# Optimization experiments

Hardware: AMD Instinct MI355X
Metric: run time of the kernel (lower is better)

Reference implementation:

```python
import jax, jax.numpy as jnp
import numpy as np

N_NODES = 100000


def _sage_conv(x, src, dst, W_l, b_l, W_r):
    # mean-aggregate neighbor (source) features at target nodes
    gathered = x[src]                                   # [E, D]
    summed = jax.ops.segment_sum(gathered, dst, num_segments=N_NODES)  # [N, D]
    deg = jax.ops.segment_sum(jnp.ones((src.shape[0],), x.dtype), dst,
                              num_segments=N_NODES)     # [N]
    mean = summed / jnp.maximum(deg, 1.0)[:, None]      # zero stays zero for isolated nodes
    # PyG SAGEConv: lin_l(aggr) + lin_r(x); bias on lin_l only
    return mean @ W_l + b_l + x @ W_r


def setup_inputs() -> dict:
    key = jax.random.key(0)
    ks = jax.random.split(key, 9)
    x = jax.random.normal(ks[0], (N_NODES, 128), dtype=jnp.float32)
    edge_index = jax.random.randint(ks[1], (2, 1600000), 0, N_NODES, dtype=jnp.int64)
    s1 = 1.0 / np.sqrt(128.0)
    s2 = 1.0 / np.sqrt(32.0)
    return {
        "x": x,
        "edge_index": edge_index,
        "W1_l": jax.random.normal(ks[2], (128, 32), jnp.float32) * s1,
        "b1_l": jax.random.normal(ks[3], (32,), jnp.float32) * s1,
        "W1_r": jax.random.normal(ks[4], (128, 32), jnp.float32) * s1,
        "W2_l": jax.random.normal(ks[5], (32, 32), jnp.float32) * s2,
        "b2_l": jax.random.normal(ks[6], (32,), jnp.float32) * s2,
        "W2_r": jax.random.normal(ks[7], (32, 32), jnp.float32) * s2,
    }


def reference(x, edge_index, W1_l, b1_l, W1_r, W2_l, b2_l, W2_r):
    src, dst = edge_index[0], edge_index[1]
    h = _sage_conv(x, src, dst, W1_l, b1_l, W1_r)
    h = jax.nn.relu(h)
    # dropout is identity in eval mode
    h = _sage_conv(h, src, dst, W2_l, b2_l, W2_r)
    return jax.nn.relu(h)
```

## Files before the change

### kernel.cpp

```cpp
#include <hip/hip_runtime.h>


typedef _Float16 f16;
typedef _Float16 f16x2 __attribute__((ext_vector_type(2)));
typedef _Float16 f16x4 __attribute__((ext_vector_type(4)));
typedef _Float16 half8 __attribute__((ext_vector_type(8)));
typedef float f32x4 __attribute__((ext_vector_type(4)));

#define MAXBINS 2048
#define SHIFT 6
#define BINSZ 64
#define CAP 48
#define GSC 256
#define BSC 512
#define SRC_BITS 17
#define SRC_MASK 0x1FFFFu
#define XSTRIDE 136


__global__ __launch_bounds__(BSC) void block_hist(const int* __restrict__ dst,
                                                  int* __restrict__ blockHist,
                                                  int E, int chunk) {
    __shared__ int sh[MAXBINS];
    for (int i = threadIdx.x; i < MAXBINS; i += BSC) sh[i] = 0;
    __syncthreads();
    int base = blockIdx.x * chunk;
    int end = base + chunk < E ? base + chunk : E;
    for (int e = base + threadIdx.x; e < end; e += BSC)
        atomicAdd(&sh[dst[e] >> SHIFT], 1);
    __syncthreads();
    for (int i = threadIdx.x; i < MAXBINS; i += BSC)
        blockHist[(size_t)blockIdx.x * MAXBINS + i] = sh[i];
}

__global__ __launch_bounds__(256) void col_scan(const int* __restrict__ blockHist,
                                                int* __restrict__ blockBaseRel,
                                                int* __restrict__ binTot) {
    const int wave = threadIdx.x >> 6;
    const int lane = threadIdx.x & 63;
    const int bin = blockIdx.x * 4 + wave;
    int carry = 0;
#pragma unroll
    for (int r = 0; r < GSC / 64; ++r) {
        int b = r * 64 + lane;
        int v = blockHist[(size_t)b * MAXBINS + bin];
        int inc = v;
#pragma unroll
        for (int off = 1; off < 64; off <<= 1) {
            int t = __shfl_up(inc, off, 64);
            if (lane >= off) inc += t;
        }
        blockBaseRel[(size_t)b * MAXBINS + bin] = carry + (inc - v);
        carry += __shfl(inc, 63, 64);
    }
    binTot[bin] = carry;
}

__global__ __launch_bounds__(1024) void scan_bins(const int* __restrict__ binTot,
                                                  int* __restrict__ binStart,
                                                  int* __restrict__ binCnt) {
    __shared__ int sh[1024];
    int t = threadIdx.x;
    int v0 = binTot[2 * t], v1 = binTot[2 * t + 1];
    sh[t] = v0 + v1;
    __syncthreads();
    for (int off = 1; off < 1024; off <<= 1) {
        int x = 0;
        if (t >= off) x = sh[t - off];
        __syncthreads();
        sh[t] += x;
        __syncthreads();
    }
    int excl = sh[t] - (v0 + v1);
    binStart[2 * t] = excl;
    binStart[2 * t + 1] = excl + v0;
    binCnt[2 * t] = v0;
    binCnt[2 * t + 1] = v1;
}

__global__ __launch_bounds__(BSC) void scatter_binned(const int* __restrict__ src,
                                                      const int* __restrict__ dst,
                                                      const int* __restrict__ blockBaseRel,
                                                      const int* __restrict__ binStart,
                                                      unsigned* __restrict__ pairs,
                                                      int E, int chunk) {
    __shared__ int cur[MAXBINS];
    for (int i = threadIdx.x; i < MAXBINS; i += BSC)
        cur[i] = blockBaseRel[(size_t)blockIdx.x * MAXBINS + i] + binStart[i];
    __syncthreads();
    int base = blockIdx.x * chunk;
    int end = base + chunk < E ? base + chunk : E;
    for (int e = base + threadIdx.x; e < end; e += BSC) {
        int s = src[e], d = dst[e];
        int slot = atomicAdd(&cur[d >> SHIFT], 1);
        pairs[slot] = ((unsigned)(d & (BINSZ - 1)) << SRC_BITS) | (unsigned)s;
    }
}


__global__ __launch_bounds__(256) void gemm_mfma(const float* __restrict__ x,
                                                 const float* __restrict__ Wl,
                                                 const float* __restrict__ Wr,
                                                 f16* __restrict__ yl,
                                                 float* __restrict__ yr,
                                                 int N) {
    __shared__ f16 sX[64 * XSTRIDE];
    __shared__ f16 sWT[64 * XSTRIDE];
    const int tid = threadIdx.x;
    const int row0 = blockIdx.x * 64;

    for (int i = tid; i < 64 * 32; i += 256) {
        int r = i >> 5, c4 = i & 31;
        int row = row0 + r;
        float4 v = make_float4(0.f, 0.f, 0.f, 0.f);
        if (row < N) v = *(const float4*)(x + (size_t)row * 128 + c4 * 4);
        f16* d = &sX[r * XSTRIDE + c4 * 4];
        d[0] = (f16)v.x; d[1] = (f16)v.y; d[2] = (f16)v.z; d[3] = (f16)v.w;
    }
    for (int i = tid; i < 64 * 128; i += 256) {
        int k = i >> 6, n = i & 63;
        float v = (n < 32) ? Wl[k * 32 + n] : Wr[k * 32 + (n - 32)];
        sWT[n * XSTRIDE + k] = (f16)v;
    }
    __syncthreads();

    const int w = tid >> 6;
    const int lane = tid & 63;
    const int l15 = lane & 15, quad = lane >> 4;
    f32x4 acc[4] = {};
#pragma unroll
    for (int kc = 0; kc < 4; ++kc) {
        half8 af = *(const half8*)&sX[(w * 16 + l15) * XSTRIDE + kc * 32 + quad * 8];
#pragma unroll
        for (int nt = 0; nt < 4; ++nt) {
            half8 bf = *(const half8*)&sWT[(nt * 16 + l15) * XSTRIDE + kc * 32 + quad * 8];
            acc[nt] = __builtin_amdgcn_mfma_f32_16x16x32_f16(af, bf, acc[nt], 0, 0, 0);
        }
    }
#pragma unroll
    for (int nt = 0; nt < 4; ++nt) {
        int c = nt * 16 + l15;
#pragma unroll
        for (int r = 0; r < 4; ++r) {
            int g = row0 + w * 16 + quad * 4 + r;
            if (g < N) {
                if (c < 32) yl[(size_t)g * 32 + c] = (f16)acc[nt][r];
                else        yr[(size_t)g * 32 + (c - 32)] = acc[nt][r];
            }
        }
    }
}


__device__ __forceinline__ void pull_pair(const int* sBucket, int n0, int n1,
                                          int m0, int m1,
                                          const f16x2* __restrict__ y2, int col2,
                                          float2* r0, float2* r1) {
    const int4* bk0 = (const int4*)&sBucket[n0 * CAP];
    const int4* bk1 = (const int4*)&sBucket[n1 * CAP];
    float a0x = 0.f, a0y = 0.f, a1x = 0.f, a1y = 0.f;
    const int q0 = m0 >> 2, q1 = m1 >> 2;
    const int qmax = q0 > q1 ? q0 : q1;
    for (int j = 0; j < qmax; ++j) {
        if (j < q0) {
            int4 a = bk0[j];
            f16x2 v0 = y2[(size_t)a.x * 16 + col2];
            f16x2 v1 = y2[(size_t)a.y * 16 + col2];
            f16x2 v2 = y2[(size_t)a.z * 16 + col2];
            f16x2 v3 = y2[(size_t)a.w * 16 + col2];
            a0x += ((float)v0[0] + (float)v1[0]) + ((float)v2[0] + (float)v3[0]);
            a0y += ((float)v0[1] + (float)v1[1]) + ((float)v2[1] + (float)v3[1]);
        }
        if (j < q1) {
            int4 a = bk1[j];
            f16x2 v0 = y2[(size_t)a.x * 16 + col2];
            f16x2 v1 = y2[(size_t)a.y * 16 + col2];
            f16x2 v2 = y2[(size_t)a.z * 16 + col2];
            f16x2 v3 = y2[(size_t)a.w * 16 + col2];
            a1x += ((float)v0[0] + (float)v1[0]) + ((float)v2[0] + (float)v3[0]);
            a1y += ((float)v0[1] + (float)v1[1]) + ((float)v2[1] + (float)v3[1]);
        }
    }
    for (int jj = q0 * 4; jj < m0; ++jj) {
        int s = sBucket[n0 * CAP + jj];
        f16x2 v = y2[(size_t)s * 16 + col2];
        a0x += (float)v[0]; a0y += (float)v[1];
    }
    for (int jj = q1 * 4; jj < m1; ++jj) {
        int s = sBucket[n1 * CAP + jj];
        f16x2 v = y2[(size_t)s * 16 + col2];
        a1x += (float)v[0]; a1y += (float)v[1];
    }
    *r0 = make_float2(a0x, a0y);
    *r1 = make_float2(a1x, a1y);
}

__global__ __launch_bounds__(256) void agg_l1(const unsigned* __restrict__ pairs,
                                              const int* __restrict__ binStart,
                                              const int* __restrict__ binCnt,
                                              const f16* __restrict__ yl,
                                              const float* __restrict__ yr,
                                              const float* __restrict__ b1,
                                              const float* __restrict__ W2l,
                                              const float* __restrict__ W2r,
                                              f16* __restrict__ zl,
                                              float* __restrict__ zr,
                                              int N) {
    __shared__ int sBucket[BINSZ * CAP];
    __shared__ int sCnt[BINSZ];
    __shared__ float sW[2048];
    __shared__ float sB[32];
    const int tid = threadIdx.x;
    if (tid < BINSZ) sCnt[tid] = 0;
    if (tid < 32) sB[tid] = b1[tid];
    for (int i = tid; i < 2048; i += 256) sW[i] = (i < 1024) ? W2l[i] : W2r[i - 1024];
    __syncthreads();

    const int b = blockIdx.x;
    const int start = binStart[b];
    const int endE = start + binCnt[b];
    for (int e = start + tid; e < endE; e += 256) {
        unsigned pk = pairs[e];
        int local = pk >> SRC_BITS;
        int slot = atomicAdd(&sCnt[local], 1);
        if (slot < CAP) sBucket[local * CAP + slot] = (int)(pk & SRC_MASK);
    }
    __syncthreads();

    const int grp = tid >> 4;
    const int col2 = tid & 15;
    const int node0 = b << SHIFT;
    const f16x2* yl2 = (const f16x2*)yl;
    const float2 bb = *(const float2*)&sB[2 * col2];

    int deg[4], mm[4];
#pragma unroll
    for (int it = 0; it < 4; ++it) {
        deg[it] = sCnt[grp + it * 16];
        mm[it] = deg[it] < CAP ? deg[it] : CAP;
    }
    float2 acc[4];
    pull_pair(sBucket, grp, grp + 32, mm[0], mm[2], yl2, col2, &acc[0], &acc[2]);
    pull_pair(sBucket, grp + 16, grp + 48, mm[1], mm[3], yl2, col2, &acc[1], &acc[3]);

    float2 hreg[4];
#pragma unroll
    for (int it = 0; it < 4; ++it) {
        int g = node0 + grp + it * 16;
        float2 hv = make_float2(0.f, 0.f);
        if (g < N) {
            float dg = deg[it] > 1 ? (float)deg[it] : 1.0f;
            float2 loc = *(const float2*)(yr + (size_t)g * 32 + 2 * col2);
            hv.x = fmaxf(acc[it].x / dg + bb.x + loc.x, 0.0f);
            hv.y = fmaxf(acc[it].y / dg + bb.y + loc.y, 0.0f);
        }
        hreg[it] = hv;
    }
    __syncthreads();

    float* sH = (float*)sBucket;
#pragma unroll
    for (int it = 0; it < 4; ++it) {
        int n = grp + it * 16;
        *(float2*)&sH[n * 34 + 2 * col2] = hreg[it];
    }
    __syncthreads();

    const int n2 = tid >> 3;
    const int cq = tid & 7;
    const float4* sW4l = (const float4*)sW;
    const float4* sW4r = (const float4*)(sW + 1024);
#pragma unroll
    for (int it = 0; it < 2; ++it) {
        int n = it * 32 + n2;
        int g = node0 + n;
        float4 al = make_float4(0.f, 0.f, 0.f, 0.f);
        float4 ar = make_float4(0.f, 0.f, 0.f, 0.f);
#pragma unroll 8
        for (int k = 0; k < 32; ++k) {
            float hk = sH[n * 34 + k];
            float4 wl = sW4l[k * 8 + cq];
            float4 wr = sW4r[k * 8 + cq];
            al.x += hk * wl.x; al.y += hk * wl.y; al.z += hk * wl.z; al.w += hk * wl.w;
            ar.x += hk * wr.x; ar.y += hk * wr.y; ar.z += hk * wr.z; ar.w += hk * wr.w;
        }
        if (g < N) {
            f16x4 h;
            h[0] = (f16)al.x; h[1] = (f16)al.y; h[2] = (f16)al.z; h[3] = (f16)al.w;
            *(f16x4*)(zl + (size_t)g * 32 + cq * 4) = h;
            *(float4*)(zr + (size_t)g * 32 + cq * 4) = ar;
        }
    }
}

__global__ __launch_bounds__(256) void agg_l2(const unsigned* __restrict__ pairs,
                                              const int* __restrict__ binStart,
                                              const int* __restrict__ binCnt,
                                              const f16* __restrict__ zl,
                                              const float* __restrict__ b2,
                                              float* __restrict__ io,
                                              int N) {
    __shared__ int sBucket[BINSZ * CAP];
    __shared__ int sCnt[BINSZ];
    __shared__ float sB[32];
    const int tid = threadIdx.x;
    if (tid < BINSZ) sCnt[tid] = 0;
    if (tid < 32) sB[tid] = b2[tid];
    __syncthreads();

    const int b = blockIdx.x;
    const int start = binStart[b];
    const int endE = start + binCnt[b];
    for (int e = start + tid; e < endE; e += 256) {
        unsigned pk = pairs[e];
        int local = pk >> SRC_BITS;
        int slot = atomicAdd(&sCnt[local], 1);
        if (slot < CAP) sBucket[local * CAP + slot] = (int)(pk & SRC_MASK);
    }
    __syncthreads();

    const int grp = tid >> 4, col2 = tid & 15;
    const int node0 = b << SHIFT;
    const f16x2* zl2 = (const f16x2*)zl;
    const float2 bb = *(const float2*)&sB[2 * col2];

    int deg[4], mm[4];
#pragma unroll
    for (int it = 0; it < 4; ++it) {
        deg[it] = sCnt[grp + it * 16];
        mm[it] = deg[it] < CAP ? deg[it] : CAP;
    }
    float2 acc[4];
    pull_pair(sBucket, grp, grp + 32, mm[0], mm[2], zl2, col2, &acc[0], &acc[2]);
    pull_pair(sBucket, grp + 16, grp + 48, mm[1], mm[3], zl2, col2, &acc[1], &acc[3]);

#pragma unroll
    for (int it = 0; it < 4; ++it) {
        int g = node0 + grp + it * 16;
        if (g >= N) continue;
        float dg = deg[it] > 1 ? (float)deg[it] : 1.0f;
        float2 io2 = *(const float2*)(io + (size_t)g * 32 + 2 * col2);
        float2 o;
        o.x = fmaxf(acc[it].x / dg + bb.x + io2.x, 0.0f);
        o.y = fmaxf(acc[it].y / dg + bb.y + io2.y, 0.0f);
        *(float2*)(io + (size_t)g * 32 + 2 * col2) = o;
    }
}

extern "C" void kernel_launch(void* const* d_in, const int* in_sizes, int n_in,
                              void* d_out, int out_size, void* d_ws, size_t ws_size,
                              hipStream_t stream) {
    const float* x    = (const float*)d_in[0];
    const int*   ei   = (const int*)d_in[1];
    const float* W1l  = (const float*)d_in[2];
    const float* b1l  = (const float*)d_in[3];
    const float* W1r  = (const float*)d_in[4];
    const float* W2l  = (const float*)d_in[5];
    const float* b2l  = (const float*)d_in[6];
    const float* W2r  = (const float*)d_in[7];

    const int N = in_sizes[0] / 128;
    const int E = in_sizes[1] / 2;
    const int* srcIdx = ei;
    const int* dstIdx = ei + E;

    const int nbins = (N + BINSZ - 1) >> SHIFT;
    const int chunk = (E + GSC - 1) / GSC;

    int*      blockHist = (int*)d_ws;
    int*      blockBase = blockHist + (size_t)GSC * MAXBINS;
    int*      binTot    = blockBase + (size_t)GSC * MAXBINS;
    int*      binStart  = binTot + MAXBINS;
    int*      binCnt    = binStart + MAXBINS;
    unsigned* pairs     = (unsigned*)(binCnt + MAXBINS);
    f16*      A         = (f16*)(pairs + E);
    float*    B         = (float*)(A + (size_t)N * 32);
    f16*      Z         = (f16*)(B + (size_t)N * 32);
    float*    outp      = (float*)d_out;

    block_hist<<<GSC, BSC, 0, stream>>>(dstIdx, blockHist, E, chunk);
    col_scan<<<MAXBINS / 4, 256, 0, stream>>>(blockHist, blockBase, binTot);
    scan_bins<<<1, 1024, 0, stream>>>(binTot, binStart, binCnt);
    scatter_binned<<<GSC, BSC, 0, stream>>>(srcIdx, dstIdx, blockBase, binStart,
                                            pairs, E, chunk);

    gemm_mfma<<<(N + 63) / 64, 256, 0, stream>>>(x, W1l, W1r, A, B, N);
    agg_l1<<<nbins, 256, 0, stream>>>(pairs, binStart, binCnt, A, B, b1l,
                                      W2l, W2r, Z, outp, N);
    agg_l2<<<nbins, 256, 0, stream>>>(pairs, binStart, binCnt, Z, b2l, outp, N);
}
```

Baseline: 223.4 us.

## Gather 16-byte neighbor rows per thread with padded buckets and sentinel row

The aggregation kernels now assign four threads per node. Each thread loads half8 (16-byte) slices of neighbor rows, replacing the earlier 16 threads per node each loading 4-byte f16x2 values. Buckets are padded to multiples of 8 with a sentinel index N, which points at an extra padded row allocated past the end of the intermediate buffers, so the inner loop has no tail handling. The GEMM grid is enlarged so that it writes the padded rows, and some bounds checks are dropped. This cuts the number of memory instructions and the per-edge overhead, but relies on padded rows being finite. It also lowers the number of threads in flight per node.

```diff
diff --git a/kernel.cpp b/kernel.cpp
--- a/kernel.cpp
+++ b/kernel.cpp
@@ -11,6 +11,7 @@
 #define SHIFT 6
 #define BINSZ 64
 #define CAP 48
+#define BSTR 52
 #define GSC 256
 #define BSC 512
 #define SRC_BITS 17
@@ -143,57 +144,12 @@
 #pragma unroll
         for (int r = 0; r < 4; ++r) {
             int g = row0 + w * 16 + quad * 4 + r;
-            if (g < N) {
-                if (c < 32) yl[(size_t)g * 32 + c] = (f16)acc[nt][r];
-                else        yr[(size_t)g * 32 + (c - 32)] = acc[nt][r];
-            }
+            if (c < 32) yl[(size_t)g * 32 + c] = (f16)acc[nt][r];
+            else        yr[(size_t)g * 32 + (c - 32)] = acc[nt][r];
         }
     }
 }
 
-
-__device__ __forceinline__ void pull_pair(const int* sBucket, int n0, int n1,
-                                          int m0, int m1,
-                                          const f16x2* __restrict__ y2, int col2,
-                                          float2* r0, float2* r1) {
-    const int4* bk0 = (const int4*)&sBucket[n0 * CAP];
-    const int4* bk1 = (const int4*)&sBucket[n1 * CAP];
-    float a0x = 0.f, a0y = 0.f, a1x = 0.f, a1y = 0.f;
-    const int q0 = m0 >> 2, q1 = m1 >> 2;
-    const int qmax = q0 > q1 ? q0 : q1;
-    for (int j = 0; j < qmax; ++j) {
-        if (j < q0) {
-            int4 a = bk0[j];
-            f16x2 v0 = y2[(size_t)a.x * 16 + col2];
-            f16x2 v1 = y2[(size_t)a.y * 16 + col2];
-            f16x2 v2 = y2[(size_t)a.z * 16 + col2];
-            f16x2 v3 = y2[(size_t)a.w * 16 + col2];
-            a0x += ((float)v0[0] + (float)v1[0]) + ((float)v2[0] + (float)v3[0]);
-            a0y += ((float)v0[1] + (float)v1[1]) + ((float)v2[1] + (float)v3[1]);
-        }
-        if (j < q1) {
-            int4 a = bk1[j];
-            f16x2 v0 = y2[(size_t)a.x * 16 + col2];
-            f16x2 v1 = y2[(size_t)a.y * 16 + col2];
-            f16x2 v2 = y2[(size_t)a.z * 16 + col2];
-            f16x2 v3 = y2[(size_t)a.w * 16 + col2];
-            a1x += ((float)v0[0] + (float)v1[0]) + ((float)v2[0] + (float)v3[0]);
-            a1y += ((float)v0[1] + (float)v1[1]) + ((float)v2[1] + (float)v3[1]);
-        }
-    }
-    for (int jj = q0 * 4; jj < m0; ++jj) {
-        int s = sBucket[n0 * CAP + jj];
-        f16x2 v = y2[(size_t)s * 16 + col2];
-        a0x += (float)v[0]; a0y += (float)v[1];
-    }
-    for (int jj = q1 * 4; jj < m1; ++jj) {
-        int s = sBucket[n1 * CAP + jj];
-        f16x2 v = y2[(size_t)s * 16 + col2];
-        a1x += (float)v[0]; a1y += (float)v[1];
-    }
-    *r0 = make_float2(a0x, a0y);
-    *r1 = make_float2(a1x, a1y);
-}
 
 __global__ __launch_bounds__(256) void agg_l1(const unsigned* __restrict__ pairs,
                                               const int* __restrict__ binStart,
@@ -206,10 +162,10 @@
                                               f16* __restrict__ zl,
                                               float* __restrict__ zr,
                                               int N) {
-    __shared__ int sBucket[BINSZ * CAP];
+    __shared__ __align__(16) int sBucket[BINSZ * BSTR];
     __shared__ int sCnt[BINSZ];
-    __shared__ float sW[2048];
-    __shared__ float sB[32];
+    __shared__ __align__(16) float sW[2048];
+    __shared__ __align__(16) float sB[32];
     const int tid = threadIdx.x;
     if (tid < BINSZ) sCnt[tid] = 0;
     if (tid < 32) sB[tid] = b1[tid];
@@ -223,47 +179,65 @@
         unsigned pk = pairs[e];
         int local = pk >> SRC_BITS;
         int slot = atomicAdd(&sCnt[local], 1);
-        if (slot < CAP) sBucket[local * CAP + slot] = (int)(pk & SRC_MASK);
-    }
-    __syncthreads();
-
-    const int grp = tid >> 4;
-    const int col2 = tid & 15;
+        if (slot < CAP) sBucket[local * BSTR + slot] = (int)(pk & SRC_MASK);
+    }
+    __syncthreads();
+
+    if (tid < BINSZ) {
+        int c = sCnt[tid];
+        int m = c < CAP ? c : CAP;
+        int mp = (m + 7) & ~7;
+        for (int k = m; k < mp; ++k) sBucket[tid * BSTR + k] = N;
+    }
+    __syncthreads();
+
+    const int node = tid >> 2;
+    const int c8 = tid & 3;
     const int node0 = b << SHIFT;
-    const f16x2* yl2 = (const f16x2*)yl;
-    const float2 bb = *(const float2*)&sB[2 * col2];
-
-    int deg[4], mm[4];
-#pragma unroll
-    for (int it = 0; it < 4; ++it) {
-        deg[it] = sCnt[grp + it * 16];
-        mm[it] = deg[it] < CAP ? deg[it] : CAP;
-    }
-    float2 acc[4];
-    pull_pair(sBucket, grp, grp + 32, mm[0], mm[2], yl2, col2, &acc[0], &acc[2]);
-    pull_pair(sBucket, grp + 16, grp + 48, mm[1], mm[3], yl2, col2, &acc[1], &acc[3]);
-
-    float2 hreg[4];
-#pragma unroll
-    for (int it = 0; it < 4; ++it) {
-        int g = node0 + grp + it * 16;
-        float2 hv = make_float2(0.f, 0.f);
-        if (g < N) {
-            float dg = deg[it] > 1 ? (float)deg[it] : 1.0f;
-            float2 loc = *(const float2*)(yr + (size_t)g * 32 + 2 * col2);
-            hv.x = fmaxf(acc[it].x / dg + bb.x + loc.x, 0.0f);
-            hv.y = fmaxf(acc[it].y / dg + bb.y + loc.y, 0.0f);
-        }
-        hreg[it] = hv;
+    const int g = node0 + node;
+
+    const int deg = sCnt[node];
+    const int m = deg < CAP ? deg : CAP;
+    const int q = (m + 7) >> 3;
+    const int4* bk = (const int4*)&sBucket[node * BSTR];
+    const f16* yb = yl + c8 * 8;
+
+    float ax[8] = {0.f, 0.f, 0.f, 0.f, 0.f, 0.f, 0.f, 0.f};
+    for (int j = 0; j < q; ++j) {
+        int4 eA = bk[2 * j];
+        int4 eB = bk[2 * j + 1];
+        half8 v0 = *(const half8*)(yb + (size_t)eA.x * 32);
+        half8 v1 = *(const half8*)(yb + (size_t)eA.y * 32);
+        half8 v2 = *(const half8*)(yb + (size_t)eA.z * 32);
+        half8 v3 = *(const half8*)(yb + (size_t)eA.w * 32);
+        half8 w0 = *(const half8*)(yb + (size_t)eB.x * 32);
+        half8 w1 = *(const half8*)(yb + (size_t)eB.y * 32);
+        half8 w2 = *(const half8*)(yb + (size_t)eB.z * 32);
+        half8 w3 = *(const half8*)(yb + (size_t)eB.w * 32);
+#pragma unroll
+        for (int k = 0; k < 8; ++k)
+            ax[k] += (((float)v0[k] + (float)v1[k]) + ((float)v2[k] + (float)v3[k]))
+                   + (((float)w0[k] + (float)w1[k]) + ((float)w2[k] + (float)w3[k]));
+    }
+
+    float h[8];
+    if (g < N) {
+        float dg = deg > 1 ? (float)deg : 1.0f;
+        float loc[8];
+        *(float4*)&loc[0] = *(const float4*)(yr + (size_t)g * 32 + c8 * 8);
+        *(float4*)&loc[4] = *(const float4*)(yr + (size_t)g * 32 + c8 * 8 + 4);
+#pragma unroll
+        for (int k = 0; k < 8; ++k)
+            h[k] = fmaxf(ax[k] / dg + sB[c8 * 8 + k] + loc[k], 0.0f);
+    } else {
+#pragma unroll
+        for (int k = 0; k < 8; ++k) h[k] = 0.f;
     }
     __syncthreads();
 
     float* sH = (float*)sBucket;
-#pragma unroll
-    for (int it = 0; it < 4; ++it) {
-        int n = grp + it * 16;
-        *(float2*)&sH[n * 34 + 2 * col2] = hreg[it];
-    }
+    *(float4*)&sH[node * 36 + c8 * 8]     = make_float4(h[0], h[1], h[2], h[3]);
+    *(float4*)&sH[node * 36 + c8 * 8 + 4] = make_float4(h[4], h[5], h[6], h[7]);
     __syncthreads();
 
     const int n2 = tid >> 3;
@@ -273,23 +247,21 @@
 #pragma unroll
     for (int it = 0; it < 2; ++it) {
         int n = it * 32 + n2;
-        int g = node0 + n;
+        int gg = node0 + n;
         float4 al = make_float4(0.f, 0.f, 0.f, 0.f);
         float4 ar = make_float4(0.f, 0.f, 0.f, 0.f);
 #pragma unroll 8
         for (int k = 0; k < 32; ++k) {
-            float hk = sH[n * 34 + k];
+            float hk = sH[n * 36 + k];
             float4 wl = sW4l[k * 8 + cq];
             float4 wr = sW4r[k * 8 + cq];
             al.x += hk * wl.x; al.y += hk * wl.y; al.z += hk * wl.z; al.w += hk * wl.w;
             ar.x += hk * wr.x; ar.y += hk * wr.y; ar.z += hk * wr.z; ar.w += hk * wr.w;
         }
-        if (g < N) {
-            f16x4 h;
-            h[0] = (f16)al.x; h[1] = (f16)al.y; h[2] = (f16)al.z; h[3] = (f16)al.w;
-            *(f16x4*)(zl + (size_t)g * 32 + cq * 4) = h;
-            *(float4*)(zr + (size_t)g * 32 + cq * 4) = ar;
-        }
+        f16x4 hh;
+        hh[0] = (f16)al.x; hh[1] = (f16)al.y; hh[2] = (f16)al.z; hh[3] = (f16)al.w;
+        *(f16x4*)(zl + (size_t)gg * 32 + cq * 4) = hh;
+        if (gg < N) *(float4*)(zr + (size_t)gg * 32 + cq * 4) = ar;
     }
 }
 
@@ -300,9 +272,9 @@
                                               const float* __restrict__ b2,
                                               float* __restrict__ io,
                                               int N) {
-    __shared__ int sBucket[BINSZ * CAP];
+    __shared__ __align__(16) int sBucket[BINSZ * BSTR];
     __shared__ int sCnt[BINSZ];
-    __shared__ float sB[32];
+    __shared__ __align__(16) float sB[32];
     const int tid = threadIdx.x;
     if (tid < BINSZ) sCnt[tid] = 0;
     if (tid < 32) sB[tid] = b2[tid];
@@ -315,35 +287,58 @@
         unsigned pk = pairs[e];
         int local = pk >> SRC_BITS;
         int slot = atomicAdd(&sCnt[local], 1);
-        if (slot < CAP) sBucket[local * CAP + slot] = (int)(pk & SRC_MASK);
-    }
-    __syncthreads();
-
-    const int grp = tid >> 4, col2 = tid & 15;
+        if (slot < CAP) sBucket[local * BSTR + slot] = (int)(pk & SRC_MASK);
+    }
+    __syncthreads();
+
+    if (tid < BINSZ) {
+        int c = sCnt[tid];
+        int m = c < CAP ? c : CAP;
+        int mp = (m + 7) & ~7;
+        for (int k = m; k < mp; ++k) sBucket[tid * BSTR + k] = N;
+    }
+    __syncthreads();
+
+    const int node = tid >> 2;
+    const int c8 = tid & 3;
     const int node0 = b << SHIFT;
-    const f16x2* zl2 = (const f16x2*)zl;
-    const float2 bb = *(const float2*)&sB[2 * col2];
-
-    int deg[4], mm[4];
-#pragma unroll
-    for (int it = 0; it < 4; ++it) {
-        deg[it] = sCnt[grp + it * 16];
-        mm[it] = deg[it] < CAP ? deg[it] : CAP;
-    }
-    float2 acc[4];
-    pull_pair(sBucket, grp, grp + 32, mm[0], mm[2], zl2, col2, &acc[0], &acc[2]);
-    pull_pair(sBucket, grp + 16, grp + 48, mm[1], mm[3], zl2, col2, &acc[1], &acc[3]);
-
-#pragma unroll
-    for (int it = 0; it < 4; ++it) {
-        int g = node0 + grp + it * 16;
-        if (g >= N) continue;
-        float dg = deg[it] > 1 ? (float)deg[it] : 1.0f;
-        float2 io2 = *(const float2*)(io + (size_t)g * 32 + 2 * col2);
-        float2 o;
-        o.x = fmaxf(acc[it].x / dg + bb.x + io2.x, 0.0f);
-        o.y = fmaxf(acc[it].y / dg + bb.y + io2.y, 0.0f);
-        *(float2*)(io + (size_t)g * 32 + 2 * col2) = o;
+    const int g = node0 + node;
+
+    const int deg = sCnt[node];
+    const int m = deg < CAP ? deg : CAP;
+    const int q = (m + 7) >> 3;
+    const int4* bk = (const int4*)&sBucket[node * BSTR];
+    const f16* zb = zl + c8 * 8;
+
+    float ax[8] = {0.f, 0.f, 0.f, 0.f, 0.f, 0.f, 0.f, 0.f};
+    for (int j = 0; j < q; ++j) {
+        int4 eA = bk[2 * j];
+        int4 eB = bk[2 * j + 1];
+        half8 v0 = *(const half8*)(zb + (size_t)eA.x * 32);
+        half8 v1 = *(const half8*)(zb + (size_t)eA.y * 32);
+        half8 v2 = *(const half8*)(zb + (size_t)eA.z * 32);
+        half8 v3 = *(const half8*)(zb + (size_t)eA.w * 32);
+        half8 w0 = *(const half8*)(zb + (size_t)eB.x * 32);
+        half8 w1 = *(const half8*)(zb + (size_t)eB.y * 32);
+        half8 w2 = *(const half8*)(zb + (size_t)eB.z * 32);
+        half8 w3 = *(const half8*)(zb + (size_t)eB.w * 32);
+#pragma unroll
+        for (int k = 0; k < 8; ++k)
+            ax[k] += (((float)v0[k] + (float)v1[k]) + ((float)v2[k] + (float)v3[k]))
+                   + (((float)w0[k] + (float)w1[k]) + ((float)w2[k] + (float)w3[k]));
+    }
+
+    if (g < N) {
+        float dg = deg > 1 ? (float)deg : 1.0f;
+        float v[8];
+        *(float4*)&v[0] = *(const float4*)(io + (size_t)g * 32 + c8 * 8);
+        *(float4*)&v[4] = *(const float4*)(io + (size_t)g * 32 + c8 * 8 + 4);
+        float o[8];
+#pragma unroll
+        for (int k = 0; k < 8; ++k)
+            o[k] = fmaxf(ax[k] / dg + sB[c8 * 8 + k] + v[k], 0.0f);
+        *(float4*)(io + (size_t)g * 32 + c8 * 8)     = *(float4*)&o[0];
+        *(float4*)(io + (size_t)g * 32 + c8 * 8 + 4) = *(float4*)&o[4];
     }
 }
 
@@ -364,6 +359,9 @@
     const int* srcIdx = ei;
     const int* dstIdx = ei + E;
 
+    const int gridG = (N >> 6) + 1;
+    const int NP = gridG << 6;
+
     const int nbins = (N + BINSZ - 1) >> SHIFT;
     const int chunk = (E + GSC - 1) / GSC;
 
@@ -374,8 +372,8 @@
     int*      binCnt    = binStart + MAXBINS;
     unsigned* pairs     = (unsigned*)(binCnt + MAXBINS);
     f16*      A         = (f16*)(pairs + E);
-    float*    B         = (float*)(A + (size_t)N * 32);
-    f16*      Z         = (f16*)(B + (size_t)N * 32);
+    float*    B         = (float*)(A + (size_t)NP * 32);
+    f16*      Z         = (f16*)(B + (size_t)NP * 32);
     float*    outp      = (float*)d_out;
 
     block_hist<<<GSC, BSC, 0, stream>>>(dstIdx, blockHist, E, chunk);
@@ -384,7 +382,7 @@
     scatter_binned<<<GSC, BSC, 0, stream>>>(srcIdx, dstIdx, blockBase, binStart,
                                             pairs, E, chunk);
 
-    gemm_mfma<<<(N + 63) / 64, 256, 0, stream>>>(x, W1l, W1r, A, B, N);
+    gemm_mfma<<<gridG, 256, 0, stream>>>(x, W1l, W1r, A, B, N);
     agg_l1<<<nbins, 256, 0, stream>>>(pairs, binStart, binCnt, A, B, b1l,
                                       W2l, W2r, Z, outp, N);
     agg_l2<<<nbins, 256, 0, stream>>>(pairs, binStart, binCnt, Z, b2l, outp, N);
```

After: 201.6 us. 9.8% less time.
